# Kernel optimization log

Hardware: AMD Instinct MI355X
Metric: run time of the kernel (lower is better)

Reference implementation:

```python
import jax, jax.numpy as jnp
import numpy as np

IN_DIMS = (8, 8, 8, 8)
OUT_DIMS = (8, 8, 8, 8)
RANKS = (1, 16, 16, 16, 1)
BATCH = 4096


def setup_inputs() -> dict:
    key = jax.random.key(0)
    ks = jax.random.split(key, 6)
    n_in = int(np.prod(IN_DIMS))
    n_out = int(np.prod(OUT_DIMS))
    d = len(IN_DIMS)
    # t3f glorot: total matrix variance 2/(n_in+n_out), split evenly across cores/ranks
    lamb = 2.0 / (n_in + n_out)
    cv = (lamb / np.prod(RANKS)) ** (1.0 / d)
    core_std = float(np.sqrt(cv))
    cores = {}
    for i in range(d):
        shp = (RANKS[i], IN_DIMS[i], OUT_DIMS[i], RANKS[i + 1])
        cores[f"core{i}"] = core_std * jax.random.normal(ks[i], shp, dtype=jnp.float32)
    x = jax.random.normal(ks[4], (BATCH, n_in), dtype=jnp.float32)
    b = 0.1 * jnp.ones((n_out,), dtype=jnp.float32)
    return {"x": x, **cores, "b": b}


def tt_dense(x, cores):
    """y = x @ M, M the TT-matrix with cores [r_{k-1}, a_k, b_k, r_k]."""
    B = x.shape[0]
    rest = int(np.prod(IN_DIMS[1:]))
    # t: [B, P(out dims done), r, a_k, rest(in dims todo)]
    t = x.reshape(B, 1, 1, IN_DIMS[0], rest)
    for k, core in enumerate(cores):
        # contract rank r and input mode a_k -> produce output mode b_k and next rank q
        t = jnp.einsum('zpras,rabq->zpbqs', t, core)
        z, p, bd, q, s = t.shape
        if k < len(cores) - 1:
            a_next = IN_DIMS[k + 1]
            t = t.reshape(z, p * bd, q, a_next, s // a_next)
        else:
            t = t.reshape(z, p * bd)  # q == s == 1
    return t  # [B, prod(OUT_DIMS)]


def reference(x, core0, core1, core2, core3, b):
    y = tt_dense(x, [core0, core1, core2, core3])
    return jax.nn.relu(y + b)
```

## Files before the change

kernel.cpp:

```cpp
#include <hip/hip_runtime.h>
#include <hip/hip_bf16.h>
#include <cstdint>
#include <cstddef>


#define GM 4096
#define GN 4096
#define GK 4096
#define NT (GK / 64)

typedef __attribute__((ext_vector_type(8))) short short8_t;
typedef __attribute__((ext_vector_type(4))) float float4_t;

__device__ __forceinline__ unsigned short f2bf(float f) {
  union { float f; uint32_t u; } v; v.f = f;
  uint32_t u = v.u;
  uint32_t r = (u + 0x7fffu + ((u >> 16) & 1u)) >> 16;
  return (unsigned short)r;
}

__global__ __launch_bounds__(256) void prep_kernel(
    const float* __restrict__ c0, const float* __restrict__ c1,
    const float* __restrict__ c2, const float* __restrict__ c3,
    float* __restrict__ G01, float* __restrict__ G23t) {
  int idx = blockIdx.x * 256 + threadIdx.x;
  if (idx < 65536) {
    int r2 = idx & 15;
    int b01 = (idx >> 4) & 63;
    int a01 = idx >> 10;
    int a0 = a01 >> 3, a1 = a01 & 7, b0 = b01 >> 3, b1 = b01 & 7;
    float s = 0.f;
#pragma unroll
    for (int r1 = 0; r1 < 16; ++r1)
      s += c0[(a0 * 8 + b0) * 16 + r1] * c1[((r1 * 8 + a1) * 8 + b1) * 16 + r2];
    G01[idx] = s;
  } else {
    int t = idx - 65536;
    int a23 = t & 63;
    int b23 = (t >> 6) & 63;
    int r2 = t >> 12;
    int a2 = a23 >> 3, a3 = a23 & 7, b2 = b23 >> 3, b3 = b23 & 7;
    float s = 0.f;
#pragma unroll
    for (int r3 = 0; r3 < 16; ++r3)
      s += c2[((r2 * 8 + a2) * 8 + b2) * 16 + r3] * c3[(r3 * 8 + a3) * 8 + b3];
    G23t[t] = s;
  }
}

__global__ __launch_bounds__(256) void mt_convert(
    const float* __restrict__ G01, const float* __restrict__ G23t,
    unsigned short* __restrict__ Mt,
    const float* __restrict__ x, unsigned short* __restrict__ xb) {
  int bid = blockIdx.x;
  int tid = threadIdx.x;
  if (bid < 1024) {
    int a01 = bid >> 4;
    int g = bid & 15;

    float acc[4][16];
#pragma unroll
    for (int j = 0; j < 4; ++j)
#pragma unroll
      for (int i = 0; i < 16; ++i) acc[j][i] = 0.f;

    for (int r2 = 0; r2 < 16; ++r2) {
      float gv[4];
#pragma unroll
      for (int j = 0; j < 4; ++j)
        gv[j] = G01[(a01 * 64 + g * 4 + j) * 16 + r2];
      const float* src = G23t + r2 * 4096 + tid * 16;
      float4_t v0 = *(const float4_t*)(src);
      float4_t v1 = *(const float4_t*)(src + 4);
      float4_t v2 = *(const float4_t*)(src + 8);
      float4_t v3 = *(const float4_t*)(src + 12);
#pragma unroll
      for (int j = 0; j < 4; ++j) {
#pragma unroll
        for (int l = 0; l < 4; ++l) {
          acc[j][l]      += gv[j] * v0[l];
          acc[j][4 + l]  += gv[j] * v1[l];
          acc[j][8 + l]  += gv[j] * v2[l];
          acc[j][12 + l] += gv[j] * v3[l];
        }
      }
    }

    int b23 = tid >> 2;
    int a23base = (tid & 3) * 16;
#pragma unroll
    for (int j = 0; j < 4; ++j) {
      short8_t o0, o1;
#pragma unroll
      for (int i = 0; i < 8; ++i) {
        o0[i] = (short)f2bf(acc[j][i]);
        o1[i] = (short)f2bf(acc[j][8 + i]);
      }
      size_t base = (size_t)((g * 4 + j) * 64 + b23) * GK + a01 * 64 + a23base;
      *(short8_t*)(Mt + base) = o0;
      *(short8_t*)(Mt + base + 8) = o1;
    }
  } else {
    int i = ((bid - 1024) * 256 + tid) * 8;
    float4_t a = *(const float4_t*)(x + i);
    float4_t b = *(const float4_t*)(x + i + 4);
    short8_t o;
    o[0] = (short)f2bf(a[0]); o[1] = (short)f2bf(a[1]);
    o[2] = (short)f2bf(a[2]); o[3] = (short)f2bf(a[3]);
    o[4] = (short)f2bf(b[0]); o[5] = (short)f2bf(b[1]);
    o[6] = (short)f2bf(b[2]); o[7] = (short)f2bf(b[3]);
    *(short8_t*)(xb + i) = o;
  }
}

__global__ __launch_bounds__(512, 2) void gemm_bias_relu(
    const unsigned short* __restrict__ A, const unsigned short* __restrict__ Bt,
    const float* __restrict__ bias, float* __restrict__ C) {
  extern __shared__ __align__(16) unsigned short lds[];

  const int tid = threadIdx.x;
  const int bswz = blockIdx.x;
  const int xcd = bswz & 7, li = bswz >> 3;
  const int row0 = ((xcd >> 1) * 4 + (li >> 3)) * 256;
  const int col0 = ((xcd & 1) * 8 + (li & 7)) * 256;
  const int wave = tid >> 6, lane = tid & 63;
  const int wm = wave >> 2, wn = wave & 3;
  const int half = lane >> 4, mrow = lane & 15;

  const int r0 = tid >> 3, p0 = tid & 7, h0 = (p0 - r0) & 7;
  const unsigned short* Abase = A + (size_t)(row0 + r0) * GK + h0 * 8;
  const unsigned short* Bbase = Bt + (size_t)(col0 + r0) * GK + h0 * 8;
  const int dA = r0 * 64 + p0 * 8;
  const int dB = dA + 16384;

#define GLD(SRC, DST)                                                  \
  __builtin_amdgcn_global_load_lds(                                    \
      (const __attribute__((address_space(1))) void*)(SRC),            \
      (__attribute__((address_space(3))) void*)(lds + (DST)), 16, 0, 0)
#define STAGE_A(G, KT, BUF)                                            \
  do {                                                                 \
    const unsigned short* s_ = Abase + (size_t)(G) * 128 * GK + (KT) * 64; \
    GLD(s_, (BUF) * 32768 + (G) * 8192 + dA);                          \
    GLD(s_ + (size_t)64 * GK, (BUF) * 32768 + (G) * 8192 + dA + 4096); \
  } while (0)
#define STAGE_B(G, KT, BUF)                                            \
  do {                                                                 \
    const unsigned short* s_ = Bbase + (size_t)(G) * 128 * GK + (KT) * 64; \
    GLD(s_, (BUF) * 32768 + (G) * 8192 + dB);                          \
    GLD(s_ + (size_t)64 * GK, (BUF) * 32768 + (G) * 8192 + dB + 4096); \
  } while (0)

  const int arow = wm * 128 + mrow;
  const int aoff0 = arow * 64 + ((half + arow) & 7) * 8;
  const int aoff1 = aoff0 ^ 32;
  const int brow = wn * 64 + mrow;
  const int boff0 = 16384 + brow * 64 + ((half + brow) & 7) * 8;
  const int boff1 = boff0 ^ 32;

  float4_t acc[8][4];
#pragma unroll
  for (int i = 0; i < 8; ++i)
#pragma unroll
    for (int n = 0; n < 4; ++n) acc[i][n] = (float4_t){0.f, 0.f, 0.f, 0.f};

  STAGE_A(0, 0, 0); STAGE_A(1, 0, 0); STAGE_B(0, 0, 0); STAGE_B(1, 0, 0);
  STAGE_B(0, 1, 1); STAGE_A(0, 1, 1); STAGE_A(1, 1, 1);
  asm volatile("s_waitcnt vmcnt(6)" ::: "memory");
  __builtin_amdgcn_s_barrier();
  __builtin_amdgcn_sched_barrier(0);

#pragma unroll 2
  for (int kt = 0; kt < NT; ++kt) {
    const int cur = kt & 1;
    const int cb = cur * 32768;

    short8_t bfr[4][2], af01[2][2], af23[2][2], af45[2][2], af67[2][2];

#pragma unroll
    for (int n = 0; n < 4; ++n) {
      bfr[n][0] = *(const short8_t*)&lds[cb + boff0 + n * 1024];
      bfr[n][1] = *(const short8_t*)&lds[cb + boff1 + n * 1024];
    }
#pragma unroll
    for (int ii = 0; ii < 2; ++ii) {
      af01[ii][0] = *(const short8_t*)&lds[cb + aoff0 + ii * 1024];
      af01[ii][1] = *(const short8_t*)&lds[cb + aoff1 + ii * 1024];
    }
    if (kt + 1 < NT) STAGE_B(1, kt + 1, cur ^ 1);
    __builtin_amdgcn_s_setprio(1);
#pragma unroll
    for (int ks = 0; ks < 2; ++ks)
#pragma unroll
      for (int ii = 0; ii < 2; ++ii)
#pragma unroll
        for (int n = 0; n < 4; ++n)
          acc[ii][n] = __builtin_amdgcn_mfma_f32_16x16x32_bf16(
              af01[ii][ks], bfr[n][ks], acc[ii][n], 0, 0, 0);
    __builtin_amdgcn_s_setprio(0);
    __builtin_amdgcn_s_barrier();
    __builtin_amdgcn_sched_barrier(0);

    if (kt + 2 < NT) STAGE_B(0, kt + 2, cur);
#pragma unroll
    for (int ii = 0; ii < 2; ++ii) {
      af23[ii][0] = *(const short8_t*)&lds[cb + aoff0 + (2 + ii) * 1024];
      af23[ii][1] = *(const short8_t*)&lds[cb + aoff1 + (2 + ii) * 1024];
    }
#pragma unroll
    for (int ii = 0; ii < 2; ++ii) {
      af45[ii][0] = *(const short8_t*)&lds[cb + aoff0 + (4 + ii) * 1024];
      af45[ii][1] = *(const short8_t*)&lds[cb + aoff1 + (4 + ii) * 1024];
      af67[ii][0] = *(const short8_t*)&lds[cb + aoff0 + (6 + ii) * 1024];
      af67[ii][1] = *(const short8_t*)&lds[cb + aoff1 + (6 + ii) * 1024];
    }
    __builtin_amdgcn_s_setprio(1);
#pragma unroll
    for (int ks = 0; ks < 2; ++ks)
#pragma unroll
      for (int ii = 0; ii < 2; ++ii)
#pragma unroll
        for (int n = 0; n < 4; ++n)
          acc[2 + ii][n] = __builtin_amdgcn_mfma_f32_16x16x32_bf16(
              af23[ii][ks], bfr[n][ks], acc[2 + ii][n], 0, 0, 0);
#pragma unroll
    for (int ks = 0; ks < 2; ++ks)
#pragma unroll
      for (int ii = 0; ii < 2; ++ii)
#pragma unroll
        for (int n = 0; n < 4; ++n)
          acc[4 + ii][n] = __builtin_amdgcn_mfma_f32_16x16x32_bf16(
              af45[ii][ks], bfr[n][ks], acc[4 + ii][n], 0, 0, 0);
    __builtin_amdgcn_s_setprio(0);
    asm volatile("s_waitcnt lgkmcnt(0)" ::: "memory");
    __builtin_amdgcn_s_barrier();
    __builtin_amdgcn_sched_barrier(0);

    if (kt + 2 < NT) { STAGE_A(0, kt + 2, cur); STAGE_A(1, kt + 2, cur); }
    __builtin_amdgcn_s_setprio(1);
#pragma unroll
    for (int ks = 0; ks < 2; ++ks)
#pragma unroll
      for (int ii = 0; ii < 2; ++ii)
#pragma unroll
        for (int n = 0; n < 4; ++n)
          acc[6 + ii][n] = __builtin_amdgcn_mfma_f32_16x16x32_bf16(
              af67[ii][ks], bfr[n][ks], acc[6 + ii][n], 0, 0, 0);
    __builtin_amdgcn_s_setprio(0);
    if (kt + 2 < NT)
      asm volatile("s_waitcnt vmcnt(6)" ::: "memory");
    else if (kt + 1 < NT)
      asm volatile("s_waitcnt vmcnt(0)" ::: "memory");
    __builtin_amdgcn_s_barrier();
    __builtin_amdgcn_sched_barrier(0);
  }

#undef STAGE_B
#undef STAGE_A
#undef GLD

#pragma unroll
  for (int n = 0; n < 4; ++n) {
    int col = col0 + wn * 64 + n * 16 + mrow;
    float bcol = bias[col];
#pragma unroll
    for (int i = 0; i < 8; ++i) {
#pragma unroll
      for (int r = 0; r < 4; ++r) {
        int row = row0 + wm * 128 + i * 16 + half * 4 + r;
        float v = acc[i][n][r] + bcol;
        C[(size_t)row * GN + col] = v > 0.f ? v : 0.f;
      }
    }
  }
}

extern "C" void kernel_launch(void* const* d_in, const int* in_sizes, int n_in,
                              void* d_out, int out_size, void* d_ws, size_t ws_size,
                              hipStream_t stream) {
  const float* x  = (const float*)d_in[0];
  const float* c0 = (const float*)d_in[1];
  const float* c1 = (const float*)d_in[2];
  const float* c2 = (const float*)d_in[3];
  const float* c3 = (const float*)d_in[4];
  const float* b  = (const float*)d_in[5];
  float* out = (float*)d_out;

  unsigned short* xb = (unsigned short*)d_ws;
  unsigned short* Mt = (unsigned short*)((char*)d_ws + (32u << 20));
  float* G01 = (float*)((char*)d_ws + (64u << 20));
  float* G23t = G01 + 65536;

  static bool lds_configured = false;
  if (!lds_configured) {
    (void)hipFuncSetAttribute((const void*)gemm_bias_relu,
                              hipFuncAttributeMaxDynamicSharedMemorySize,
                              131072);
    lds_configured = true;
  }

  prep_kernel<<<512, 256, 0, stream>>>(c0, c1, c2, c3, G01, G23t);
  mt_convert<<<1024 + (GM * GK) / (256 * 8), 256, 0, stream>>>(
      G01, G23t, Mt, x, xb);
  gemm_bias_relu<<<(GM / 256) * (GN / 256), 512, 131072, stream>>>(
      xb, Mt, b, out);
}
```

Before: 247.0 us.

## Restructure GEMM main loop into ping-pong A-fragment register prefetch schedule

New measurement: 252.9 us. +2.4%, slower.

```diff
diff --git a/kernel.cpp b/kernel.cpp
--- a/kernel.cpp
+++ b/kernel.cpp
@@ -157,103 +157,109 @@
   const int boff0 = 16384 + brow * 64 + ((half + brow) & 7) * 8;
   const int boff1 = boff0 ^ 32;
 
+#define RD_A(DST, BUF, Q)                                                   \
+  do {                                                                      \
+    _Pragma("unroll")                                                       \
+    for (int ii = 0; ii < 2; ++ii) {                                        \
+      DST[ii * 2 + 0] =                                                     \
+          *(const short8_t*)&lds[(BUF)*32768 + aoff0 + (2*(Q)+ii) * 1024];  \
+      DST[ii * 2 + 1] =                                                     \
+          *(const short8_t*)&lds[(BUF)*32768 + aoff1 + (2*(Q)+ii) * 1024];  \
+    }                                                                       \
+  } while (0)
+#define RD_B(DST, BUF)                                                      \
+  do {                                                                      \
+    _Pragma("unroll")                                                       \
+    for (int n = 0; n < 4; ++n) {                                           \
+      DST[n * 2 + 0] =                                                      \
+          *(const short8_t*)&lds[(BUF)*32768 + boff0 + n * 1024];           \
+      DST[n * 2 + 1] =                                                      \
+          *(const short8_t*)&lds[(BUF)*32768 + boff1 + n * 1024];           \
+    }                                                                       \
+  } while (0)
+#define MFMA_Q(Q, AF, BV)                                                   \
+  do {                                                                      \
+    __builtin_amdgcn_s_setprio(1);                                          \
+    _Pragma("unroll")                                                       \
+    for (int ks = 0; ks < 2; ++ks)                                          \
+      _Pragma("unroll")                                                     \
+      for (int ii = 0; ii < 2; ++ii)                                        \
+        _Pragma("unroll")                                                   \
+        for (int n = 0; n < 4; ++n)                                         \
+          acc[2*(Q)+ii][n] = __builtin_amdgcn_mfma_f32_16x16x32_bf16(       \
+              AF[ii * 2 + ks], BV[n * 2 + ks], acc[2*(Q)+ii][n], 0, 0, 0);  \
+    __builtin_amdgcn_s_setprio(0);                                          \
+  } while (0)
+#define BAR()                                                               \
+  do {                                                                      \
+    __builtin_amdgcn_s_barrier();                                           \
+    __builtin_amdgcn_sched_barrier(0);                                      \
+  } while (0)
+
   float4_t acc[8][4];
 #pragma unroll
   for (int i = 0; i < 8; ++i)
 #pragma unroll
     for (int n = 0; n < 4; ++n) acc[i][n] = (float4_t){0.f, 0.f, 0.f, 0.f};
 
+  short8_t b0v[8], b1v[8], afE[4], afO[4];
+
   STAGE_A(0, 0, 0); STAGE_A(1, 0, 0); STAGE_B(0, 0, 0); STAGE_B(1, 0, 0);
-  STAGE_B(0, 1, 1); STAGE_A(0, 1, 1); STAGE_A(1, 1, 1);
-  asm volatile("s_waitcnt vmcnt(6)" ::: "memory");
-  __builtin_amdgcn_s_barrier();
-  __builtin_amdgcn_sched_barrier(0);
-
-#pragma unroll 2
-  for (int kt = 0; kt < NT; ++kt) {
-    const int cur = kt & 1;
-    const int cb = cur * 32768;
-
-    short8_t bfr[4][2], af01[2][2], af23[2][2], af45[2][2], af67[2][2];
-
-#pragma unroll
-    for (int n = 0; n < 4; ++n) {
-      bfr[n][0] = *(const short8_t*)&lds[cb + boff0 + n * 1024];
-      bfr[n][1] = *(const short8_t*)&lds[cb + boff1 + n * 1024];
-    }
-#pragma unroll
-    for (int ii = 0; ii < 2; ++ii) {
-      af01[ii][0] = *(const short8_t*)&lds[cb + aoff0 + ii * 1024];
-      af01[ii][1] = *(const short8_t*)&lds[cb + aoff1 + ii * 1024];
-    }
-    if (kt + 1 < NT) STAGE_B(1, kt + 1, cur ^ 1);
-    __builtin_amdgcn_s_setprio(1);
-#pragma unroll
-    for (int ks = 0; ks < 2; ++ks)
-#pragma unroll
-      for (int ii = 0; ii < 2; ++ii)
-#pragma unroll
-        for (int n = 0; n < 4; ++n)
-          acc[ii][n] = __builtin_amdgcn_mfma_f32_16x16x32_bf16(
-              af01[ii][ks], bfr[n][ks], acc[ii][n], 0, 0, 0);
-    __builtin_amdgcn_s_setprio(0);
-    __builtin_amdgcn_s_barrier();
-    __builtin_amdgcn_sched_barrier(0);
-
-    if (kt + 2 < NT) STAGE_B(0, kt + 2, cur);
-#pragma unroll
-    for (int ii = 0; ii < 2; ++ii) {
-      af23[ii][0] = *(const short8_t*)&lds[cb + aoff0 + (2 + ii) * 1024];
-      af23[ii][1] = *(const short8_t*)&lds[cb + aoff1 + (2 + ii) * 1024];
-    }
-#pragma unroll
-    for (int ii = 0; ii < 2; ++ii) {
-      af45[ii][0] = *(const short8_t*)&lds[cb + aoff0 + (4 + ii) * 1024];
-      af45[ii][1] = *(const short8_t*)&lds[cb + aoff1 + (4 + ii) * 1024];
-      af67[ii][0] = *(const short8_t*)&lds[cb + aoff0 + (6 + ii) * 1024];
-      af67[ii][1] = *(const short8_t*)&lds[cb + aoff1 + (6 + ii) * 1024];
-    }
-    __builtin_amdgcn_s_setprio(1);
-#pragma unroll
-    for (int ks = 0; ks < 2; ++ks)
-#pragma unroll
-      for (int ii = 0; ii < 2; ++ii)
-#pragma unroll
-        for (int n = 0; n < 4; ++n)
-          acc[2 + ii][n] = __builtin_amdgcn_mfma_f32_16x16x32_bf16(
-              af23[ii][ks], bfr[n][ks], acc[2 + ii][n], 0, 0, 0);
-#pragma unroll
-    for (int ks = 0; ks < 2; ++ks)
-#pragma unroll
-      for (int ii = 0; ii < 2; ++ii)
-#pragma unroll
-        for (int n = 0; n < 4; ++n)
-          acc[4 + ii][n] = __builtin_amdgcn_mfma_f32_16x16x32_bf16(
-              af45[ii][ks], bfr[n][ks], acc[4 + ii][n], 0, 0, 0);
-    __builtin_amdgcn_s_setprio(0);
-    asm volatile("s_waitcnt lgkmcnt(0)" ::: "memory");
-    __builtin_amdgcn_s_barrier();
-    __builtin_amdgcn_sched_barrier(0);
-
-    if (kt + 2 < NT) { STAGE_A(0, kt + 2, cur); STAGE_A(1, kt + 2, cur); }
-    __builtin_amdgcn_s_setprio(1);
-#pragma unroll
-    for (int ks = 0; ks < 2; ++ks)
-#pragma unroll
-      for (int ii = 0; ii < 2; ++ii)
-#pragma unroll
-        for (int n = 0; n < 4; ++n)
-          acc[6 + ii][n] = __builtin_amdgcn_mfma_f32_16x16x32_bf16(
-              af67[ii][ks], bfr[n][ks], acc[6 + ii][n], 0, 0, 0);
-    __builtin_amdgcn_s_setprio(0);
+  STAGE_B(0, 1, 1); STAGE_B(1, 1, 1);
+  asm volatile("s_waitcnt vmcnt(4)" ::: "memory");
+  BAR();
+  RD_B(b0v, 0);
+  RD_A(afE, 0, 0);
+
+  for (int kt = 0; kt < NT; kt += 2) {
+    RD_A(afO, 0, 1);
+    STAGE_A(0, kt + 1, 1);
+    MFMA_Q(0, afE, b0v);
+    BAR();
+    RD_A(afE, 0, 2);
+    STAGE_A(1, kt + 1, 1);
+    if (kt + 2 < NT) STAGE_B(0, kt + 2, 0);
+    MFMA_Q(1, afO, b0v);
+    BAR();
+    RD_A(afO, 0, 3);
+    if (kt + 2 < NT) STAGE_B(1, kt + 2, 0);
+    MFMA_Q(2, afE, b0v);
     if (kt + 2 < NT)
-      asm volatile("s_waitcnt vmcnt(6)" ::: "memory");
-    else if (kt + 1 < NT)
+      asm volatile("s_waitcnt vmcnt(4)" ::: "memory");
+    else
       asm volatile("s_waitcnt vmcnt(0)" ::: "memory");
-    __builtin_amdgcn_s_barrier();
-    __builtin_amdgcn_sched_barrier(0);
-  }
-
+    BAR();
+    RD_B(b1v, 1);
+    RD_A(afE, 1, 0);
+    MFMA_Q(3, afO, b0v);
+    BAR();
+
+    RD_A(afO, 1, 1);
+    if (kt + 2 < NT) STAGE_A(0, kt + 2, 0);
+    MFMA_Q(0, afE, b1v);
+    BAR();
+    RD_A(afE, 1, 2);
+    if (kt + 2 < NT) STAGE_A(1, kt + 2, 0);
+    if (kt + 3 < NT) STAGE_B(0, kt + 3, 1);
+    MFMA_Q(1, afO, b1v);
+    BAR();
+    RD_A(afO, 1, 3);
+    if (kt + 3 < NT) STAGE_B(1, kt + 3, 1);
+    MFMA_Q(2, afE, b1v);
+    if (kt + 3 < NT)
+      asm volatile("s_waitcnt vmcnt(4)" ::: "memory");
+    else
+      asm volatile("s_waitcnt vmcnt(0)" ::: "memory");
+    BAR();
+    if (kt + 2 < NT) { RD_B(b0v, 0); RD_A(afE, 0, 0); }
+    MFMA_Q(3, afO, b1v);
+    BAR();
+  }
+
+#undef BAR
+#undef MFMA_Q
+#undef RD_B
+#undef RD_A
 #undef STAGE_B
 #undef STAGE_A
 #undef GLD
```

## Shrink GEMM tile to 256x128 with BK=32 triple-buffered single-barrier pipeline

Applied to the files above, without the earlier changes.

Result: slower. 264.8 us (+7.2%).

```diff
diff --git a/kernel.cpp b/kernel.cpp
--- a/kernel.cpp
+++ b/kernel.cpp
@@ -7,7 +7,8 @@
 #define GM 4096
 #define GN 4096
 #define GK 4096
-#define NT (GK / 64)
+#define NT2 (GK / 32)
+#define BUFS 12288
 
 typedef __attribute__((ext_vector_type(8))) short short8_t;
 typedef __attribute__((ext_vector_type(4))) float float4_t;
@@ -113,7 +114,7 @@
   }
 }
 
-__global__ __launch_bounds__(512, 2) void gemm_bias_relu(
+__global__ __launch_bounds__(256, 2) void gemm_bias_relu(
     const unsigned short* __restrict__ A, const unsigned short* __restrict__ Bt,
     const float* __restrict__ bias, float* __restrict__ C) {
   extern __shared__ __align__(16) unsigned short lds[];
@@ -121,41 +122,40 @@
   const int tid = threadIdx.x;
   const int bswz = blockIdx.x;
   const int xcd = bswz & 7, li = bswz >> 3;
-  const int row0 = ((xcd >> 1) * 4 + (li >> 3)) * 256;
-  const int col0 = ((xcd & 1) * 8 + (li & 7)) * 256;
+  const int row0 = ((xcd >> 2) * 8 + (li >> 3)) * 256;
+  const int col0 = ((xcd & 3) * 8 + (li & 7)) * 128;
   const int wave = tid >> 6, lane = tid & 63;
-  const int wm = wave >> 2, wn = wave & 3;
+  const int wm = wave >> 1, wn = wave & 1;
   const int half = lane >> 4, mrow = lane & 15;
 
-  const int r0 = tid >> 3, p0 = tid & 7, h0 = (p0 - r0) & 7;
-  const unsigned short* Abase = A + (size_t)(row0 + r0) * GK + h0 * 8;
-  const unsigned short* Bbase = Bt + (size_t)(col0 + r0) * GK + h0 * 8;
-  const int dA = r0 * 64 + p0 * 8;
-  const int dB = dA + 16384;
+  const int rA = tid >> 2;
+  const int h0 = ((tid & 3) - (tid >> 3)) & 3;
+  const unsigned short* Ap[4];
+  const unsigned short* Bp[2];
+#pragma unroll
+  for (int q = 0; q < 4; ++q)
+    Ap[q] = A + (size_t)(row0 + q * 64 + rA) * GK + h0 * 8;
+#pragma unroll
+  for (int q = 0; q < 2; ++q)
+    Bp[q] = Bt + (size_t)(col0 + q * 64 + rA) * GK + h0 * 8;
+  const int dstA = tid * 8;
+  const int dstB = 8192 + tid * 8;
 
 #define GLD(SRC, DST)                                                  \
   __builtin_amdgcn_global_load_lds(                                    \
       (const __attribute__((address_space(1))) void*)(SRC),            \
       (__attribute__((address_space(3))) void*)(lds + (DST)), 16, 0, 0)
-#define STAGE_A(G, KT, BUF)                                            \
+#define STAGE(KT, WB)                                                  \
   do {                                                                 \
-    const unsigned short* s_ = Abase + (size_t)(G) * 128 * GK + (KT) * 64; \
-    GLD(s_, (BUF) * 32768 + (G) * 8192 + dA);                          \
-    GLD(s_ + (size_t)64 * GK, (BUF) * 32768 + (G) * 8192 + dA + 4096); \
+    _Pragma("unroll")                                                  \
+    for (int q = 0; q < 4; ++q) GLD(Ap[q] + (KT) * 32, (WB) + q * 2048 + dstA); \
+    _Pragma("unroll")                                                  \
+    for (int q = 0; q < 2; ++q) GLD(Bp[q] + (KT) * 32, (WB) + q * 2048 + dstB); \
   } while (0)
-#define STAGE_B(G, KT, BUF)                                            \
-  do {                                                                 \
-    const unsigned short* s_ = Bbase + (size_t)(G) * 128 * GK + (KT) * 64; \
-    GLD(s_, (BUF) * 32768 + (G) * 8192 + dB);                          \
-    GLD(s_ + (size_t)64 * GK, (BUF) * 32768 + (G) * 8192 + dB + 4096); \
-  } while (0)
-
-  const int arow = wm * 128 + mrow;
-  const int aoff0 = arow * 64 + ((half + arow) & 7) * 8;
-  const int aoff1 = aoff0 ^ 32;
-  const int brow = wn * 64 + mrow;
-  const int boff0 = 16384 + brow * 64 + ((half + brow) & 7) * 8;
-  const int boff1 = boff0 ^ 32;
+
+  const int pfrag = ((half + (mrow >> 1)) & 3) * 8;
+  const int aoffB = (wm * 128 + mrow) * 32 + pfrag;
+  const int boffB = 8192 + (wn * 64 + mrow) * 32 + pfrag;
 
   float4_t acc[8][4];
 #pragma unroll
@@ -163,99 +163,46 @@
 #pragma unroll
     for (int n = 0; n < 4; ++n) acc[i][n] = (float4_t){0.f, 0.f, 0.f, 0.f};
 
-  STAGE_A(0, 0, 0); STAGE_A(1, 0, 0); STAGE_B(0, 0, 0); STAGE_B(1, 0, 0);
-  STAGE_B(0, 1, 1); STAGE_A(0, 1, 1); STAGE_A(1, 1, 1);
+  STAGE(0, 0);
+  STAGE(1, BUFS);
   asm volatile("s_waitcnt vmcnt(6)" ::: "memory");
   __builtin_amdgcn_s_barrier();
   __builtin_amdgcn_sched_barrier(0);
 
-#pragma unroll 2
-  for (int kt = 0; kt < NT; ++kt) {
-    const int cur = kt & 1;
-    const int cb = cur * 32768;
-
-    short8_t bfr[4][2], af01[2][2], af23[2][2], af45[2][2], af67[2][2];
-
-#pragma unroll
-    for (int n = 0; n < 4; ++n) {
-      bfr[n][0] = *(const short8_t*)&lds[cb + boff0 + n * 1024];
-      bfr[n][1] = *(const short8_t*)&lds[cb + boff1 + n * 1024];
-    }
-#pragma unroll
-    for (int ii = 0; ii < 2; ++ii) {
-      af01[ii][0] = *(const short8_t*)&lds[cb + aoff0 + ii * 1024];
-      af01[ii][1] = *(const short8_t*)&lds[cb + aoff1 + ii * 1024];
-    }
-    if (kt + 1 < NT) STAGE_B(1, kt + 1, cur ^ 1);
+  int rb = 0;
+  int wb = 2 * BUFS;
+  for (int t = 0; t < NT2; ++t) {
+    if (t + 2 < NT2) STAGE(t + 2, wb);
+
+    short8_t af[8], bf[4];
+#pragma unroll
+    for (int m = 0; m < 8; ++m)
+      af[m] = *(const short8_t*)&lds[rb + aoffB + m * 512];
+#pragma unroll
+    for (int n = 0; n < 4; ++n)
+      bf[n] = *(const short8_t*)&lds[rb + boffB + n * 512];
+
     __builtin_amdgcn_s_setprio(1);
 #pragma unroll
-    for (int ks = 0; ks < 2; ++ks)
-#pragma unroll
-      for (int ii = 0; ii < 2; ++ii)
-#pragma unroll
-        for (int n = 0; n < 4; ++n)
-          acc[ii][n] = __builtin_amdgcn_mfma_f32_16x16x32_bf16(
-              af01[ii][ks], bfr[n][ks], acc[ii][n], 0, 0, 0);
+    for (int m = 0; m < 8; ++m)
+#pragma unroll
+      for (int n = 0; n < 4; ++n)
+        acc[m][n] = __builtin_amdgcn_mfma_f32_16x16x32_bf16(
+            af[m], bf[n], acc[m][n], 0, 0, 0);
     __builtin_amdgcn_s_setprio(0);
-    __builtin_amdgcn_s_barrier();
-    __builtin_amdgcn_sched_barrier(0);
-
-    if (kt + 2 < NT) STAGE_B(0, kt + 2, cur);
-#pragma unroll
-    for (int ii = 0; ii < 2; ++ii) {
-      af23[ii][0] = *(const short8_t*)&lds[cb + aoff0 + (2 + ii) * 1024];
-      af23[ii][1] = *(const short8_t*)&lds[cb + aoff1 + (2 + ii) * 1024];
-    }
-#pragma unroll
-    for (int ii = 0; ii < 2; ++ii) {
-      af45[ii][0] = *(const short8_t*)&lds[cb + aoff0 + (4 + ii) * 1024];
-      af45[ii][1] = *(const short8_t*)&lds[cb + aoff1 + (4 + ii) * 1024];
-      af67[ii][0] = *(const short8_t*)&lds[cb + aoff0 + (6 + ii) * 1024];
-      af67[ii][1] = *(const short8_t*)&lds[cb + aoff1 + (6 + ii) * 1024];
-    }
-    __builtin_amdgcn_s_setprio(1);
-#pragma unroll
-    for (int ks = 0; ks < 2; ++ks)
-#pragma unroll
-      for (int ii = 0; ii < 2; ++ii)
-#pragma unroll
-        for (int n = 0; n < 4; ++n)
-          acc[2 + ii][n] = __builtin_amdgcn_mfma_f32_16x16x32_bf16(
-              af23[ii][ks], bfr[n][ks], acc[2 + ii][n], 0, 0, 0);
-#pragma unroll
-    for (int ks = 0; ks < 2; ++ks)
-#pragma unroll
-      for (int ii = 0; ii < 2; ++ii)
-#pragma unroll
-        for (int n = 0; n < 4; ++n)
-          acc[4 + ii][n] = __builtin_amdgcn_mfma_f32_16x16x32_bf16(
-              af45[ii][ks], bfr[n][ks], acc[4 + ii][n], 0, 0, 0);
-    __builtin_amdgcn_s_setprio(0);
-    asm volatile("s_waitcnt lgkmcnt(0)" ::: "memory");
-    __builtin_amdgcn_s_barrier();
-    __builtin_amdgcn_sched_barrier(0);
-
-    if (kt + 2 < NT) { STAGE_A(0, kt + 2, cur); STAGE_A(1, kt + 2, cur); }
-    __builtin_amdgcn_s_setprio(1);
-#pragma unroll
-    for (int ks = 0; ks < 2; ++ks)
-#pragma unroll
-      for (int ii = 0; ii < 2; ++ii)
-#pragma unroll
-        for (int n = 0; n < 4; ++n)
-          acc[6 + ii][n] = __builtin_amdgcn_mfma_f32_16x16x32_bf16(
-              af67[ii][ks], bfr[n][ks], acc[6 + ii][n], 0, 0, 0);
-    __builtin_amdgcn_s_setprio(0);
-    if (kt + 2 < NT)
+
+    if (t + 2 < NT2)
       asm volatile("s_waitcnt vmcnt(6)" ::: "memory");
-    else if (kt + 1 < NT)
+    else if (t + 1 < NT2)
       asm volatile("s_waitcnt vmcnt(0)" ::: "memory");
     __builtin_amdgcn_s_barrier();
     __builtin_amdgcn_sched_barrier(0);
-  }
-
-#undef STAGE_B
-#undef STAGE_A
+
+    rb = (rb == 2 * BUFS) ? 0 : rb + BUFS;
+    wb = (wb == 2 * BUFS) ? 0 : wb + BUFS;
+  }
+
+#undef STAGE
 #undef GLD
 
 #pragma unroll
@@ -294,13 +241,13 @@
   if (!lds_configured) {
     (void)hipFuncSetAttribute((const void*)gemm_bias_relu,
                               hipFuncAttributeMaxDynamicSharedMemorySize,
-                              131072);
+                              3 * BUFS * 2);
     lds_configured = true;
   }
 
   prep_kernel<<<512, 256, 0, stream>>>(c0, c1, c2, c3, G01, G23t);
   mt_convert<<<1024 + (GM * GK) / (256 * 8), 256, 0, stream>>>(
       G01, G23t, Mt, x, xb);
-  gemm_bias_relu<<<(GM / 256) * (GN / 256), 512, 131072, stream>>>(
+  gemm_bias_relu<<<(GM / 256) * (GN / 128), 256, 3 * BUFS * 2, stream>>>(
       xb, Mt, b, out);
 }
```
